# Optimization experiments

Measured on AMD Instinct MI355X. Metric: run time of the kernel, lower is better.

The kernel has to match this reference:

```python
import jax, jax.numpy as jnp
import numpy as np


def _diag_gather(x):
    # out[b,c,h,w] = x[b,c,h,(h+w)%W]; then transpose last two dims and flatten
    B, C, H, W = x.shape
    idx = (jnp.arange(H)[:, None] + jnp.arange(W)[None, :]) % W
    g = jnp.take_along_axis(x, idx[None, None], axis=3)  # [B,C,H,W]
    return g.transpose(0, 1, 3, 2).reshape(B, C, H * W)


def _antidiag_gather(x):
    B, C, H, W = x.shape
    idx = (jnp.arange(W)[None, :] - jnp.arange(H)[:, None]) % W
    g = jnp.take_along_axis(x, idx[None, None], axis=3)
    return g.transpose(0, 1, 3, 2).reshape(B, C, H * W)


def _diag_scatter(flat, shape):
    # exact inverse of _diag_gather (per-row circular-shift permutation)
    B, C, H, W = shape
    t = flat.reshape(B, C, W, H).transpose(0, 1, 3, 2)  # [B,C,H,W]
    inv = (jnp.arange(W)[None, :] - jnp.arange(H)[:, None]) % W
    return jnp.take_along_axis(t, inv[None, None], axis=3)


def _antidiag_scatter(flat, shape):
    B, C, H, W = shape
    t = flat.reshape(B, C, W, H).transpose(0, 1, 3, 2)
    inv = (jnp.arange(W)[None, :] + jnp.arange(H)[:, None]) % W
    return jnp.take_along_axis(t, inv[None, None], axis=3)


def cross_scan(x):
    # x: [B,C,H,W] -> xs: [B,8,C,L]; 8 scan directions (row, col, flips, diag, antidiag, flips)
    B, C, H, W = x.shape
    L = H * W
    xf = x.reshape(B, C, L)
    xt = x.transpose(0, 1, 3, 2).reshape(B, C, L)
    xd = _diag_gather(x)
    xa = _antidiag_gather(x)
    return jnp.stack(
        [xf, xt, xf[..., ::-1], xt[..., ::-1], xd, xa, xd[..., ::-1], xa[..., ::-1]],
        axis=1,
    )


def cross_merge(ys):
    # ys: [B,8,D,H,W] -> y: [B,D,L]
    B, K, D, H, W = ys.shape
    L = H * W
    ys = ys.reshape(B, K, D, L)
    a = ys[:, 0:2] + ys[:, 2:4][..., ::-1]
    y = a[:, 0] + a[:, 1].reshape(B, D, W, H).transpose(0, 1, 3, 2).reshape(B, D, L)
    b = ys[:, 4:6] + ys[:, 6:8][..., ::-1]
    y = y + _diag_scatter(b[:, 0], (B, D, H, W)).reshape(B, D, L)
    y = y + _antidiag_scatter(b[:, 1], (B, D, H, W)).reshape(B, D, L)
    return y


def selective_scan(u, delta, A, Bs, Cs, Ds):
    # u, delta: [B,KD,L]; A: [KD,N]; Bs, Cs: [B,K,N,L]; Ds: [KD]
    Bn, KD, L = u.shape
    K = Bs.shape[1]
    Dd = KD // K
    N = A.shape[1]
    dA = jnp.exp(delta[:, :, None, :] * A[None, :, :, None])  # [B,KD,N,L]
    Bexp = jnp.broadcast_to(Bs[:, :, None], (Bn, K, Dd, N, L)).reshape(Bn, KD, N, L)
    Cexp = jnp.broadcast_to(Cs[:, :, None], (Bn, K, Dd, N, L)).reshape(Bn, KD, N, L)
    dBu = delta[:, :, None, :] * Bexp * u[:, :, None, :]

    def comb(c1, c2):
        a1, b1 = c1
        a2, b2 = c2
        return a2 * a1, a2 * b1 + b2

    _, h = jax.lax.associative_scan(comb, (dA, dBu), axis=-1)  # h: [B,KD,N,L]
    return jnp.sum(Cexp * h, axis=2) + Ds[None, :, None] * u


def setup_inputs() -> dict:
    key = jax.random.key(0)
    ks = jax.random.split(key, 8)
    B, D, H, W = 1, 96, 64, 64
    K, N, R = 8, 16, 6
    return {
        "x": jax.random.normal(ks[0], (B, D, H, W), jnp.float32),
        "x_proj_weight": jax.random.normal(ks[1], (K, R + 2 * N, D), jnp.float32) * 0.05,
        "dt_projs_weight": jax.random.normal(ks[2], (K, D, R), jnp.float32) * 0.1,
        "dt_projs_bias": jax.random.normal(ks[3], (K, D), jnp.float32) * 0.1,
        "A_logs": jax.random.uniform(ks[4], (K * D, N), jnp.float32),
        "Ds": jax.random.normal(ks[5], (K * D,), jnp.float32),
        "out_norm_weight": jnp.ones((D,), jnp.float32),
        "out_norm_bias": jnp.zeros((D,), jnp.float32),
    }


def reference(x, x_proj_weight, dt_projs_weight, dt_projs_bias, A_logs, Ds,
              out_norm_weight, out_norm_bias):
    B, D, H, W = x.shape
    K, _, R = dt_projs_weight.shape
    N = A_logs.shape[1]
    L = H * W

    xs = cross_scan(x)  # [B,K,D,L]
    x_dbl = jnp.einsum("bkdl,kcd->bkcl", xs, x_proj_weight)  # [B,K,R+2N,L]
    dts, Bs, Cs = jnp.split(x_dbl, [R, R + N], axis=2)
    dts = jnp.einsum("bkrl,kdr->bkdl", dts, dt_projs_weight)  # [B,K,D,L]

    u = xs.reshape(B, K * D, L)
    delta = jax.nn.softplus(dts.reshape(B, K * D, L)
                            + dt_projs_bias.reshape(-1)[None, :, None])
    A = -jnp.exp(A_logs)  # [KD,N]

    ys = selective_scan(u, delta, A, Bs, Cs, Ds)  # [B,KD,L]
    y = cross_merge(ys.reshape(B, K, D, H, W))  # [B,D,L]

    # out_norm (v0): LayerNorm over channel dim
    y = y.transpose(0, 2, 1)  # [B,L,D]
    mu = jnp.mean(y, axis=-1, keepdims=True)
    var = jnp.var(y, axis=-1, keepdims=True)
    y = (y - mu) * jax.lax.rsqrt(var + 1e-5) * out_norm_weight + out_norm_bias
    return y.reshape(B, H, W, D)
```

## Files before the change

kernel.cpp:

```cpp
#include <hip/hip_runtime.h>
#include <math.h>

#define D_ 96
#define L_ 4096
#define K_ 8
#define N_ 16
#define R_ 6
#define CDBL 38
#define DL_ (D_ * L_)

#define REPN(M) M(0) M(1) M(2) M(3) M(4) M(5) M(6) M(7) \
                M(8) M(9) M(10) M(11) M(12) M(13) M(14) M(15)
#define REP8(M) M(0) M(1) M(2) M(3) M(4) M(5) M(6) M(7)
#define FENCE asm volatile("" ::: "memory");

#if __has_builtin(__builtin_amdgcn_exp2f)
#define EXP2(x) __builtin_amdgcn_exp2f(x)
#else
#define EXP2(x) exp2f(x)
#endif
#if __has_builtin(__builtin_amdgcn_logf)
#define LOG2F(x) __builtin_amdgcn_logf(x)
#else
#define LOG2F(x) __log2f(x)
#endif

#define LOG2E 1.44269504088896340736f
#define LN2F  0.69314718055994530942f

__device__ __forceinline__ int src_index(int k, int l) {
    int h = l & 63, w = l >> 6;
    int lp = 4095 - l;
    int hp = lp & 63, wp = lp >> 6;
    switch (k) {
    case 0: return l;
    case 1: return (h << 6) + w;
    case 2: return lp;
    case 3: return (hp << 6) + wp;
    case 4: return (h << 6) + ((h + w) & 63);
    case 5: return (h << 6) + ((w - h) & 63);
    case 6: return (hp << 6) + ((hp + wp) & 63);
    default: return (hp << 6) + ((wp - hp) & 63);
    }
}

__global__ __launch_bounds__(256) void k_xdbl(const float* __restrict__ x,
                                              const float* __restrict__ wproj,
                                              float* __restrict__ xdbl) {
    __shared__ float tile[64][100];
    int bid = blockIdx.x;
    int swz = (bid & 7) * 64 + (bid >> 3);
    int k = swz >> 6;
    int l0 = (swz & 63) * 64;

    for (int e = threadIdx.x; e < D_ * 64; e += 256) {
        int d = e >> 6, li = e & 63;
        tile[li][d] = x[d * L_ + src_index(k, l0 + li)];
    }
    __syncthreads();

    int lt = threadIdx.x & 63;
    int cg = __builtin_amdgcn_readfirstlane(threadIdx.x >> 6);
    const float* wk = wproj + k * CDBL * D_;
    float acc[10];
    #pragma unroll
    for (int j = 0; j < 10; ++j) acc[j] = 0.f;
    for (int d4 = 0; d4 < D_; d4 += 4) {
        float4 tv = *(const float4*)&tile[lt][d4];
        #pragma unroll
        for (int j = 0; j < 10; ++j) {
            int c = cg + 4 * j;
            if (c < CDBL) {
                float4 wv = *(const float4*)&wk[c * D_ + d4];
                acc[j] = fmaf(tv.x, wv.x, acc[j]);
                acc[j] = fmaf(tv.y, wv.y, acc[j]);
                acc[j] = fmaf(tv.z, wv.z, acc[j]);
                acc[j] = fmaf(tv.w, wv.w, acc[j]);
            }
        }
    }
    #pragma unroll
    for (int j = 0; j < 10; ++j) {
        int c = cg + 4 * j;
        if (c < CDBL) xdbl[(k * CDBL + c) * L_ + l0 + lt] = acc[j];
    }
}


#if __has_builtin(__builtin_amdgcn_update_dpp)
#define HAVE_DPP 1
template<int CTRL, int RM>
__device__ __forceinline__ float updpp(float oldv, float src) {
    int r = __builtin_amdgcn_update_dpp(__builtin_bit_cast(int, oldv),
                                        __builtin_bit_cast(int, src),
                                        CTRL, RM, 0xF, false);
    return __builtin_bit_cast(float, r);
}
#else
#define HAVE_DPP 0
#endif

__global__ __launch_bounds__(512, 3) void k_scan(const float* __restrict__ xdbl,
                                                 const float* __restrict__ dtw,
                                                 const float* __restrict__ dtb,
                                                 const float* __restrict__ alogs,
                                                 const float* __restrict__ dsv_,
                                                 const float* __restrict__ x,
                                                 float* __restrict__ ys) {
    int bid = blockIdx.x;
    int k = bid & 7;
    int d = bid >> 3;
    int kd = k * D_ + d;
    int t = threadIdx.x;
    int lane = t & 63, wv = t >> 6;
    int l0t = t * 8;

    __shared__ float An_s[16];
    __shared__ float agg_a[8][16], agg_b[8][16];
    __shared__ float cb_s[8][16];
    if (t < 16)
        An_s[t] = -expf(alogs[kd * N_ + t]);

#define DECL(n) float sA##n, sB##n;
    REPN(DECL)
#undef DECL
#define DECL(i) float d##i, u##i, y##i;
    REP8(DECL)
#undef DECL

    const float* xr = xdbl + k * CDBL * L_;
    const float2* wp2 = (const float2*)(dtw + kd * R_);
    const float2 w01 = wp2[0], w23 = wp2[1], w45 = wp2[2];
    const float bias = dtb[kd];
    const float dval = dsv_[kd];
#define SPL2(dst, s) { float p = (s) * LOG2E; \
    float l2 = LOG2F(1.f + EXP2(p)); \
    dst = ((s) > 20.f) ? p : l2; }
#define DLTQ(j, i0, i1, i2, i3) { \
    const float4 r0 = *(const float4*)(xr + 0 * L_ + l0t + j * 4); \
    const float4 r1 = *(const float4*)(xr + 1 * L_ + l0t + j * 4); \
    const float4 r2 = *(const float4*)(xr + 2 * L_ + l0t + j * 4); \
    const float4 r3 = *(const float4*)(xr + 3 * L_ + l0t + j * 4); \
    const float4 r4 = *(const float4*)(xr + 4 * L_ + l0t + j * 4); \
    const float4 r5 = *(const float4*)(xr + 5 * L_ + l0t + j * 4); \
    float s; \
    s = fmaf(w01.x, r0.x, bias); s = fmaf(w01.y, r1.x, s); s = fmaf(w23.x, r2.x, s); \
    s = fmaf(w23.y, r3.x, s); s = fmaf(w45.x, r4.x, s); s = fmaf(w45.y, r5.x, s); \
    SPL2(d##i0, s) \
    s = fmaf(w01.x, r0.y, bias); s = fmaf(w01.y, r1.y, s); s = fmaf(w23.x, r2.y, s); \
    s = fmaf(w23.y, r3.y, s); s = fmaf(w45.x, r4.y, s); s = fmaf(w45.y, r5.y, s); \
    SPL2(d##i1, s) \
    s = fmaf(w01.x, r0.z, bias); s = fmaf(w01.y, r1.z, s); s = fmaf(w23.x, r2.z, s); \
    s = fmaf(w23.y, r3.z, s); s = fmaf(w45.x, r4.z, s); s = fmaf(w45.y, r5.z, s); \
    SPL2(d##i2, s) \
    s = fmaf(w01.x, r0.w, bias); s = fmaf(w01.y, r1.w, s); s = fmaf(w23.x, r2.w, s); \
    s = fmaf(w23.y, r3.w, s); s = fmaf(w45.x, r4.w, s); s = fmaf(w45.y, r5.w, s); \
    SPL2(d##i3, s) }
    DLTQ(0, 0, 1, 2, 3)
    DLTQ(1, 4, 5, 6, 7)
#undef DLTQ
#undef SPL2

    const float* xd = x + d * L_;
#define UG(i) u##i = xd[src_index(k, l0t + i)]; y##i = dval * u##i; \
    u##i *= LN2F; u##i *= d##i;
    REP8(UG)
#undef UG

    __syncthreads();

    const float* Bptr = xdbl + (k * CDBL + R_) * L_ + l0t;
    const float* Cptr = Bptr + N_ * L_;

#define PHA_E(i, Bc) { float e = EXP2(d##i * An); \
    rb = fmaf(e, rb, u##i * (Bc)); ra *= e; }
#define PHA(n) { \
    const float An = An_s[n]; \
    const float* Bn = Bptr + n * L_; \
    const float4 b0 = *(const float4*)(Bn), b1 = *(const float4*)(Bn + 4); \
    float ra = 1.f, rb = 0.f; \
    PHA_E(0, b0.x) PHA_E(1, b0.y) PHA_E(2, b0.z) PHA_E(3, b0.w) \
    PHA_E(4, b1.x) PHA_E(5, b1.y) PHA_E(6, b1.z) PHA_E(7, b1.w) \
    sA##n = ra; sB##n = rb; }
    PHA(0) PHA(1) PHA(2) PHA(3) FENCE
    PHA(4) PHA(5) PHA(6) PHA(7) FENCE
    PHA(8) PHA(9) PHA(10) PHA(11) FENCE
    PHA(12) PHA(13) PHA(14) PHA(15) FENCE
#undef PHA
#undef PHA_E

#if HAVE_DPP
#define SSTN(n) { float pa = updpp<SC_CTRL, SC_RM>(1.f, sA##n); \
                  float pb = updpp<SC_CTRL, SC_RM>(0.f, sB##n); \
                  sB##n = fmaf(sA##n, pb, sB##n); sA##n *= pa; }
#define SC_CTRL 0x111
#define SC_RM 0xF
    REPN(SSTN)
#undef SC_CTRL
#undef SC_RM
#define SC_CTRL 0x112
#define SC_RM 0xF
    REPN(SSTN)
#undef SC_CTRL
#undef SC_RM
#define SC_CTRL 0x114
#define SC_RM 0xF
    REPN(SSTN)
#undef SC_CTRL
#undef SC_RM
#define SC_CTRL 0x118
#define SC_RM 0xF
    REPN(SSTN)
#undef SC_CTRL
#undef SC_RM
#define SC_CTRL 0x142
#define SC_RM 0xA
    REPN(SSTN)
#undef SC_CTRL
#undef SC_RM
#define SC_CTRL 0x143
#define SC_RM 0xC
    REPN(SSTN)
#undef SC_CTRL
#undef SC_RM
#undef SSTN

#define PPREF(n) { \
    if (lane == 63) { agg_a[wv][n] = sA##n; agg_b[wv][n] = sB##n; } \
    sA##n = updpp<0x138, 0xF>(1.f, sA##n); \
    sB##n = updpp<0x138, 0xF>(0.f, sB##n); }
    REPN(PPREF)
#undef PPREF
#else
#define PBF(n) { float pa = __shfl_up(sA##n, off); float pb = __shfl_up(sB##n, off); \
    if (lane >= off) { sB##n = fmaf(sA##n, pb, sB##n); sA##n *= pa; } }
    for (int off = 1; off < 64; off <<= 1) { REPN(PBF) }
#undef PBF
#define PPREF(n) { float ia = sA##n, ib = sB##n; \
    float ea = __shfl_up(ia, 1); float eb = __shfl_up(ib, 1); \
    if (lane == 0) { ea = 1.f; eb = 0.f; } \
    if (lane == 63) { agg_a[wv][n] = ia; agg_b[wv][n] = ib; } \
    sA##n = ea; sB##n = eb; }
    REPN(PPREF)
#undef PPREF
#endif
    __syncthreads();

    if (t < 128) {
        int w = t >> 4, n = t & 15;
        float cb = 0.f;
        for (int w2 = 0; w2 < w; ++w2)
            cb = fmaf(agg_a[w2][n], cb, agg_b[w2][n]);
        cb_s[w][n] = cb;
    }
    __syncthreads();
#define PC(n) { sA##n = fmaf(sA##n, cb_s[wv][n], sB##n); }
    REPN(PC)
#undef PC

#define PHD_E(i, Bc, Cc) { float e = EXP2(d##i * An); \
    h = fmaf(e, h, u##i * (Bc)); y##i = fmaf((Cc), h, y##i); }
#define PHD(n) { \
    const float An = An_s[n]; float h = sA##n; \
    const float* Bn = Bptr + n * L_; const float* Cn = Cptr + n * L_; \
    const float4 b0 = *(const float4*)(Bn), b1 = *(const float4*)(Bn + 4); \
    const float4 c0 = *(const float4*)(Cn), c1 = *(const float4*)(Cn + 4); \
    PHD_E(0, b0.x, c0.x) PHD_E(1, b0.y, c0.y) PHD_E(2, b0.z, c0.z) PHD_E(3, b0.w, c0.w) \
    PHD_E(4, b1.x, c1.x) PHD_E(5, b1.y, c1.y) PHD_E(6, b1.z, c1.z) PHD_E(7, b1.w, c1.w) }
    PHD(0) PHD(1) FENCE
    PHD(2) PHD(3) FENCE
    PHD(4) PHD(5) FENCE
    PHD(6) PHD(7) FENCE
    PHD(8) PHD(9) FENCE
    PHD(10) PHD(11) FENCE
    PHD(12) PHD(13) FENCE
    PHD(14) PHD(15) FENCE
#undef PHD
#undef PHD_E

    float* yp = ys + kd * L_ + l0t;
    {
        float4 o;
        o.x = y0; o.y = y1; o.z = y2; o.w = y3; *(float4*)(yp + 0) = o;
        o.x = y4; o.y = y5; o.z = y6; o.w = y7; *(float4*)(yp + 4) = o;
    }
}

__global__ __launch_bounds__(256) void k_merge_ln(const float* __restrict__ ys,
                                                  const float* __restrict__ gamma,
                                                  const float* __restrict__ beta,
                                                  float* __restrict__ out) {
    __shared__ float sm[32][D_ + 1];
    __shared__ float mu_s[32], rs_s[32];
    int l0 = blockIdx.x * 32;
    for (int e = threadIdx.x; e < 32 * D_; e += 256) {
        int li = e & 31, d = e >> 5;
        int l = l0 + li;
        int h = l >> 6, w = l & 63;
        int i1 = (w << 6) + h;
        int i4 = (((w - h) & 63) << 6) + h;
        int i5 = (((w + h) & 63) << 6) + h;
        const float* bd = ys + d * L_;
        float v = bd[0 * DL_ + l] + bd[2 * DL_ + 4095 - l]
                + bd[1 * DL_ + i1] + bd[3 * DL_ + 4095 - i1]
                + bd[4 * DL_ + i4] + bd[6 * DL_ + 4095 - i4]
                + bd[5 * DL_ + i5] + bd[7 * DL_ + 4095 - i5];
        sm[li][d] = v;
    }
    __syncthreads();
    int li2 = threadIdx.x >> 3, sub = threadIdx.x & 7;
    float s = 0.f, sq = 0.f;
    for (int d = sub; d < D_; d += 8) {
        float v = sm[li2][d];
        s += v; sq = fmaf(v, v, sq);
    }
    s += __shfl_xor(s, 1); sq += __shfl_xor(sq, 1);
    s += __shfl_xor(s, 2); sq += __shfl_xor(sq, 2);
    s += __shfl_xor(s, 4); sq += __shfl_xor(sq, 4);
    if (sub == 0) {
        float mu = s * (1.f / 96.f);
        float var = sq * (1.f / 96.f) - mu * mu;
        mu_s[li2] = mu;
        rs_s[li2] = rsqrtf(var + 1e-5f);
    }
    __syncthreads();
    for (int e = threadIdx.x; e < 32 * D_; e += 256) {
        int li = e / D_, d = e - li * D_;
        float v = (sm[li][d] - mu_s[li]) * rs_s[li];
        out[(l0 + li) * D_ + d] = fmaf(v, gamma[d], beta[d]);
    }
}

extern "C" void kernel_launch(void* const* d_in, const int* in_sizes, int n_in,
                              void* d_out, int out_size, void* d_ws, size_t ws_size,
                              hipStream_t stream) {
    const float* x     = (const float*)d_in[0];
    const float* wproj = (const float*)d_in[1];
    const float* dtw   = (const float*)d_in[2];
    const float* dtb   = (const float*)d_in[3];
    const float* alogs = (const float*)d_in[4];
    const float* dsv   = (const float*)d_in[5];
    const float* gamma = (const float*)d_in[6];
    const float* beta  = (const float*)d_in[7];
    float* out = (float*)d_out;
    float* ws  = (float*)d_ws;

    float* xdbl = ws;
    float* ysb  = ws + 1245184;

    hipLaunchKernelGGL(k_xdbl, dim3(512), dim3(256), 0, stream, x, wproj, xdbl);
    hipLaunchKernelGGL(k_scan, dim3(768), dim3(512), 0, stream,
                       xdbl, dtw, dtb, alogs, dsv, x, ysb);
    hipLaunchKernelGGL(k_merge_ln, dim3(128), dim3(256), 0, stream,
                       ysb, gamma, beta, out);
}
```

Before: 104.0 us.

## Materialize cross-scan via LDS, split scan state in halves, separate merge and layernorm

Adds a k_xscan kernel that stages each channel image in shared memory and writes all eight scan-direction copies contiguously. k_xdbl and k_scan can then read u with coalesced float4 loads instead of scattered gathers. The scan now processes the 16 states in two halves of 8, which lowers register pressure and raises the occupancy hint from 3 to 4. The fused merge+LN kernel is split into an LDS-based merge kernel and a separate LayerNorm kernel. In exchange there are two extra launches and extra global traffic for the xs and ym buffers. k_scan also writes ys in place over xs, which is safe only because each block reads its own row before writing it.

```diff
diff --git a/kernel.cpp b/kernel.cpp
--- a/kernel.cpp
+++ b/kernel.cpp
@@ -9,8 +9,6 @@
 #define CDBL 38
 #define DL_ (D_ * L_)
 
-#define REPN(M) M(0) M(1) M(2) M(3) M(4) M(5) M(6) M(7) \
-                M(8) M(9) M(10) M(11) M(12) M(13) M(14) M(15)
 #define REP8(M) M(0) M(1) M(2) M(3) M(4) M(5) M(6) M(7)
 #define FENCE asm volatile("" ::: "memory");
 
@@ -44,7 +42,49 @@
     }
 }
 
-__global__ __launch_bounds__(256) void k_xdbl(const float* __restrict__ x,
+__device__ __forceinline__ int merge_src(int k, int l) {
+    int h = l >> 6, w = l & 63;
+    int i1 = (w << 6) + h;
+    int i4 = (((w - h) & 63) << 6) + h;
+    int i5 = (((w + h) & 63) << 6) + h;
+    switch (k) {
+    case 0: return l;
+    case 1: return i1;
+    case 2: return 4095 - l;
+    case 3: return 4095 - i1;
+    case 4: return i4;
+    case 5: return i5;
+    case 6: return 4095 - i4;
+    default: return 4095 - i5;
+    }
+}
+
+#define PQ(p) ((((p) >> 6) * 66) + ((p) & 63))
+
+__global__ __launch_bounds__(512) void k_xscan(const float* __restrict__ x,
+                                               float* __restrict__ xs) {
+    __shared__ float img[64 * 66];
+    int d = blockIdx.x;
+    int t = threadIdx.x;
+    const float* xd = x + d * L_;
+    #pragma unroll
+    for (int i = 0; i < 8; ++i) {
+        int l = i * 512 + t;
+        img[PQ(l)] = xd[l];
+    }
+    __syncthreads();
+    #pragma unroll
+    for (int k = 0; k < K_; ++k) {
+        float* dst = xs + (k * D_ + d) * L_;
+        #pragma unroll
+        for (int i = 0; i < 8; ++i) {
+            int l = i * 512 + t;
+            dst[l] = img[PQ(src_index(k, l))];
+        }
+    }
+}
+
+__global__ __launch_bounds__(256) void k_xdbl(const float* __restrict__ xs,
                                               const float* __restrict__ wproj,
                                               float* __restrict__ xdbl) {
     __shared__ float tile[64][100];
@@ -53,9 +93,10 @@
     int k = swz >> 6;
     int l0 = (swz & 63) * 64;
 
+    const float* src = xs + k * DL_ + l0;
     for (int e = threadIdx.x; e < D_ * 64; e += 256) {
         int d = e >> 6, li = e & 63;
-        tile[li][d] = x[d * L_ + src_index(k, l0 + li)];
+        tile[li][d] = src[d * L_ + li];
     }
     __syncthreads();
 
@@ -100,12 +141,12 @@
 #define HAVE_DPP 0
 #endif
 
-__global__ __launch_bounds__(512, 3) void k_scan(const float* __restrict__ xdbl,
+__global__ __launch_bounds__(512, 4) void k_scan(const float* __restrict__ xdbl,
                                                  const float* __restrict__ dtw,
                                                  const float* __restrict__ dtb,
                                                  const float* __restrict__ alogs,
                                                  const float* __restrict__ dsv_,
-                                                 const float* __restrict__ x,
+                                                 const float* __restrict__ xs,
                                                  float* __restrict__ ys) {
     int bid = blockIdx.x;
     int k = bid & 7;
@@ -116,14 +157,13 @@
     int l0t = t * 8;
 
     __shared__ float An_s[16];
-    __shared__ float agg_a[8][16], agg_b[8][16];
-    __shared__ float cb_s[8][16];
+    __shared__ float agg_a[8][8], agg_b[8][8];
+    __shared__ float cb_s[8][8];
     if (t < 16)
         An_s[t] = -expf(alogs[kd * N_ + t]);
 
-#define DECL(n) float sA##n, sB##n;
-    REPN(DECL)
-#undef DECL
+    float sA0, sA1, sA2, sA3, sA4, sA5, sA6, sA7;
+    float sB0, sB1, sB2, sB3, sB4, sB5, sB6, sB7;
 #define DECL(i) float d##i, u##i, y##i;
     REP8(DECL)
 #undef DECL
@@ -161,9 +201,14 @@
 #undef DLTQ
 #undef SPL2
 
-    const float* xd = x + d * L_;
-#define UG(i) u##i = xd[src_index(k, l0t + i)]; y##i = dval * u##i; \
-    u##i *= LN2F; u##i *= d##i;
+    {
+        const float* up = xs + kd * L_ + l0t;
+        const float4 ua = *(const float4*)(up);
+        const float4 ub = *(const float4*)(up + 4);
+        u0 = ua.x; u1 = ua.y; u2 = ua.z; u3 = ua.w;
+        u4 = ub.x; u5 = ub.y; u6 = ub.z; u7 = ub.w;
+    }
+#define UG(i) y##i = dval * u##i; u##i *= LN2F; u##i *= d##i;
     REP8(UG)
 #undef UG
 
@@ -174,109 +219,80 @@
 
 #define PHA_E(i, Bc) { float e = EXP2(d##i * An); \
     rb = fmaf(e, rb, u##i * (Bc)); ra *= e; }
-#define PHA(n) { \
-    const float An = An_s[n]; \
-    const float* Bn = Bptr + n * L_; \
+#define PHA(n, NOFF) { \
+    const float An = An_s[(NOFF) + (n)]; \
+    const float* Bn = Bptr + ((NOFF) + (n)) * L_; \
     const float4 b0 = *(const float4*)(Bn), b1 = *(const float4*)(Bn + 4); \
     float ra = 1.f, rb = 0.f; \
     PHA_E(0, b0.x) PHA_E(1, b0.y) PHA_E(2, b0.z) PHA_E(3, b0.w) \
     PHA_E(4, b1.x) PHA_E(5, b1.y) PHA_E(6, b1.z) PHA_E(7, b1.w) \
     sA##n = ra; sB##n = rb; }
-    PHA(0) PHA(1) PHA(2) PHA(3) FENCE
-    PHA(4) PHA(5) PHA(6) PHA(7) FENCE
-    PHA(8) PHA(9) PHA(10) PHA(11) FENCE
-    PHA(12) PHA(13) PHA(14) PHA(15) FENCE
-#undef PHA
-#undef PHA_E
 
 #if HAVE_DPP
-#define SSTN(n) { float pa = updpp<SC_CTRL, SC_RM>(1.f, sA##n); \
-                  float pb = updpp<SC_CTRL, SC_RM>(0.f, sB##n); \
-                  sB##n = fmaf(sA##n, pb, sB##n); sA##n *= pa; }
-#define SC_CTRL 0x111
-#define SC_RM 0xF
-    REPN(SSTN)
-#undef SC_CTRL
-#undef SC_RM
-#define SC_CTRL 0x112
-#define SC_RM 0xF
-    REPN(SSTN)
-#undef SC_CTRL
-#undef SC_RM
-#define SC_CTRL 0x114
-#define SC_RM 0xF
-    REPN(SSTN)
-#undef SC_CTRL
-#undef SC_RM
-#define SC_CTRL 0x118
-#define SC_RM 0xF
-    REPN(SSTN)
-#undef SC_CTRL
-#undef SC_RM
-#define SC_CTRL 0x142
-#define SC_RM 0xA
-    REPN(SSTN)
-#undef SC_CTRL
-#undef SC_RM
-#define SC_CTRL 0x143
-#define SC_RM 0xC
-    REPN(SSTN)
-#undef SC_CTRL
-#undef SC_RM
-#undef SSTN
-
+#define SSTAGE(CTRL, RM, n) { float pa = updpp<CTRL, RM>(1.f, sA##n); \
+    float pb = updpp<CTRL, RM>(0.f, sB##n); \
+    sB##n = fmaf(sA##n, pb, sB##n); sA##n *= pa; }
+#define SSTAGE8(CTRL, RM) \
+    SSTAGE(CTRL, RM, 0) SSTAGE(CTRL, RM, 1) SSTAGE(CTRL, RM, 2) SSTAGE(CTRL, RM, 3) \
+    SSTAGE(CTRL, RM, 4) SSTAGE(CTRL, RM, 5) SSTAGE(CTRL, RM, 6) SSTAGE(CTRL, RM, 7)
 #define PPREF(n) { \
     if (lane == 63) { agg_a[wv][n] = sA##n; agg_b[wv][n] = sB##n; } \
     sA##n = updpp<0x138, 0xF>(1.f, sA##n); \
     sB##n = updpp<0x138, 0xF>(0.f, sB##n); }
-    REPN(PPREF)
-#undef PPREF
+#define SCAN_CORE \
+    SSTAGE8(0x111, 0xF) SSTAGE8(0x112, 0xF) SSTAGE8(0x114, 0xF) SSTAGE8(0x118, 0xF) \
+    SSTAGE8(0x142, 0xA) SSTAGE8(0x143, 0xC) \
+    REP8(PPREF)
 #else
 #define PBF(n) { float pa = __shfl_up(sA##n, off); float pb = __shfl_up(sB##n, off); \
     if (lane >= off) { sB##n = fmaf(sA##n, pb, sB##n); sA##n *= pa; } }
-    for (int off = 1; off < 64; off <<= 1) { REPN(PBF) }
-#undef PBF
 #define PPREF(n) { float ia = sA##n, ib = sB##n; \
     float ea = __shfl_up(ia, 1); float eb = __shfl_up(ib, 1); \
     if (lane == 0) { ea = 1.f; eb = 0.f; } \
     if (lane == 63) { agg_a[wv][n] = ia; agg_b[wv][n] = ib; } \
     sA##n = ea; sB##n = eb; }
-    REPN(PPREF)
-#undef PPREF
+#define SCAN_CORE \
+    for (int off = 1; off < 64; off <<= 1) { REP8(PBF) } \
+    REP8(PPREF)
 #endif
-    __syncthreads();
-
-    if (t < 128) {
-        int w = t >> 4, n = t & 15;
-        float cb = 0.f;
-        for (int w2 = 0; w2 < w; ++w2)
-            cb = fmaf(agg_a[w2][n], cb, agg_b[w2][n]);
-        cb_s[w][n] = cb;
-    }
-    __syncthreads();
+
 #define PC(n) { sA##n = fmaf(sA##n, cb_s[wv][n], sB##n); }
-    REPN(PC)
-#undef PC
+#define SCAN_MID \
+    SCAN_CORE \
+    __syncthreads(); \
+    if (t < 64) { int cw = t >> 3, cn = t & 7; float cb = 0.f; \
+        for (int w2 = 0; w2 < cw; ++w2) \
+            cb = fmaf(agg_a[w2][cn], cb, agg_b[w2][cn]); \
+        cb_s[cw][cn] = cb; } \
+    __syncthreads(); \
+    REP8(PC)
 
 #define PHD_E(i, Bc, Cc) { float e = EXP2(d##i * An); \
     h = fmaf(e, h, u##i * (Bc)); y##i = fmaf((Cc), h, y##i); }
-#define PHD(n) { \
-    const float An = An_s[n]; float h = sA##n; \
-    const float* Bn = Bptr + n * L_; const float* Cn = Cptr + n * L_; \
+#define PHD(n, NOFF) { \
+    const float An = An_s[(NOFF) + (n)]; float h = sA##n; \
+    const float* Bn = Bptr + ((NOFF) + (n)) * L_; \
+    const float* Cn = Cptr + ((NOFF) + (n)) * L_; \
     const float4 b0 = *(const float4*)(Bn), b1 = *(const float4*)(Bn + 4); \
     const float4 c0 = *(const float4*)(Cn), c1 = *(const float4*)(Cn + 4); \
     PHD_E(0, b0.x, c0.x) PHD_E(1, b0.y, c0.y) PHD_E(2, b0.z, c0.z) PHD_E(3, b0.w, c0.w) \
     PHD_E(4, b1.x, c1.x) PHD_E(5, b1.y, c1.y) PHD_E(6, b1.z, c1.z) PHD_E(7, b1.w, c1.w) }
-    PHD(0) PHD(1) FENCE
-    PHD(2) PHD(3) FENCE
-    PHD(4) PHD(5) FENCE
-    PHD(6) PHD(7) FENCE
-    PHD(8) PHD(9) FENCE
-    PHD(10) PHD(11) FENCE
-    PHD(12) PHD(13) FENCE
-    PHD(14) PHD(15) FENCE
-#undef PHD
-#undef PHD_E
+
+    PHA(0, 0) PHA(1, 0) PHA(2, 0) PHA(3, 0) FENCE
+    PHA(4, 0) PHA(5, 0) PHA(6, 0) PHA(7, 0) FENCE
+    SCAN_MID
+    PHD(0, 0) PHD(1, 0) FENCE
+    PHD(2, 0) PHD(3, 0) FENCE
+    PHD(4, 0) PHD(5, 0) FENCE
+    PHD(6, 0) PHD(7, 0) FENCE
+
+    PHA(0, 8) PHA(1, 8) PHA(2, 8) PHA(3, 8) FENCE
+    PHA(4, 8) PHA(5, 8) PHA(6, 8) PHA(7, 8) FENCE
+    SCAN_MID
+    PHD(0, 8) PHD(1, 8) FENCE
+    PHD(2, 8) PHD(3, 8) FENCE
+    PHD(4, 8) PHD(5, 8) FENCE
+    PHD(6, 8) PHD(7, 8) FENCE
 
     float* yp = ys + kd * L_ + l0t;
     {
@@ -286,48 +302,80 @@
     }
 }
 
-__global__ __launch_bounds__(256) void k_merge_ln(const float* __restrict__ ys,
-                                                  const float* __restrict__ gamma,
-                                                  const float* __restrict__ beta,
-                                                  float* __restrict__ out) {
-    __shared__ float sm[32][D_ + 1];
-    __shared__ float mu_s[32], rs_s[32];
-    int l0 = blockIdx.x * 32;
-    for (int e = threadIdx.x; e < 32 * D_; e += 256) {
-        int li = e & 31, d = e >> 5;
-        int l = l0 + li;
-        int h = l >> 6, w = l & 63;
-        int i1 = (w << 6) + h;
-        int i4 = (((w - h) & 63) << 6) + h;
-        int i5 = (((w + h) & 63) << 6) + h;
-        const float* bd = ys + d * L_;
-        float v = bd[0 * DL_ + l] + bd[2 * DL_ + 4095 - l]
-                + bd[1 * DL_ + i1] + bd[3 * DL_ + 4095 - i1]
-                + bd[4 * DL_ + i4] + bd[6 * DL_ + 4095 - i4]
-                + bd[5 * DL_ + i5] + bd[7 * DL_ + 4095 - i5];
-        sm[li][d] = v;
-    }
-    __syncthreads();
-    int li2 = threadIdx.x >> 3, sub = threadIdx.x & 7;
-    float s = 0.f, sq = 0.f;
-    for (int d = sub; d < D_; d += 8) {
-        float v = sm[li2][d];
-        s += v; sq = fmaf(v, v, sq);
-    }
-    s += __shfl_xor(s, 1); sq += __shfl_xor(sq, 1);
-    s += __shfl_xor(s, 2); sq += __shfl_xor(sq, 2);
-    s += __shfl_xor(s, 4); sq += __shfl_xor(sq, 4);
-    if (sub == 0) {
+__global__ __launch_bounds__(512) void k_merge(const float* __restrict__ ys,
+                                               float* __restrict__ ym) {
+    __shared__ float buf[64 * 66];
+    int d = blockIdx.x;
+    int t = threadIdx.x;
+    float a0 = 0.f, a1 = 0.f, a2 = 0.f, a3 = 0.f,
+          a4 = 0.f, a5 = 0.f, a6 = 0.f, a7 = 0.f;
+    #pragma unroll
+    for (int k = 0; k < K_; ++k) {
+        const float* srow = ys + (k * D_ + d) * L_;
+        #pragma unroll
+        for (int i = 0; i < 8; ++i) {
+            int l = i * 512 + t;
+            buf[PQ(l)] = srow[l];
+        }
+        __syncthreads();
+#define MACC(i) { int l = i * 512 + t; a##i += buf[PQ(merge_src(k, l))]; }
+        REP8(MACC)
+#undef MACC
+        __syncthreads();
+    }
+    float* drow = ym + d * L_;
+#define MST(i) drow[i * 512 + t] = a##i;
+    REP8(MST)
+#undef MST
+}
+
+__global__ __launch_bounds__(512) void k_ln(const float* __restrict__ ym,
+                                            const float* __restrict__ gamma,
+                                            const float* __restrict__ beta,
+                                            float* __restrict__ out) {
+    __shared__ float tile[D_ * 65];
+    __shared__ float pS[8][64], pQ[8][64];
+    __shared__ float mu_s[64], rs_s[64];
+    int t = threadIdx.x;
+    int lb = blockIdx.x * 64;
+
+    #pragma unroll
+    for (int i = 0; i < 12; ++i) {
+        int e = i * 512 + t;
+        int dd = e >> 6, l_loc = e & 63;
+        tile[dd * 65 + l_loc] = ym[dd * L_ + lb + l_loc];
+    }
+    __syncthreads();
+
+    {
+        int wgrp = t >> 6, l_loc = t & 63;
+        float s = 0.f, sq = 0.f;
+        #pragma unroll
+        for (int j = 0; j < 12; ++j) {
+            float v = tile[(wgrp * 12 + j) * 65 + l_loc];
+            s += v; sq = fmaf(v, v, sq);
+        }
+        pS[wgrp][l_loc] = s; pQ[wgrp][l_loc] = sq;
+    }
+    __syncthreads();
+    if (t < 64) {
+        float s = 0.f, sq = 0.f;
+        #pragma unroll
+        for (int w2 = 0; w2 < 8; ++w2) { s += pS[w2][t]; sq += pQ[w2][t]; }
         float mu = s * (1.f / 96.f);
         float var = sq * (1.f / 96.f) - mu * mu;
-        mu_s[li2] = mu;
-        rs_s[li2] = rsqrtf(var + 1e-5f);
-    }
-    __syncthreads();
-    for (int e = threadIdx.x; e < 32 * D_; e += 256) {
-        int li = e / D_, d = e - li * D_;
-        float v = (sm[li][d] - mu_s[li]) * rs_s[li];
-        out[(l0 + li) * D_ + d] = fmaf(v, gamma[d], beta[d]);
+        mu_s[t] = mu;
+        rs_s[t] = rsqrtf(var + 1e-5f);
+    }
+    __syncthreads();
+
+    #pragma unroll
+    for (int i = 0; i < 12; ++i) {
+        int e = i * 512 + t;
+        int l_loc = e / 96, dd = e - l_loc * 96;
+        float v = tile[dd * 65 + l_loc];
+        float o = fmaf((v - mu_s[l_loc]) * rs_s[l_loc], gamma[dd], beta[dd]);
+        out[lb * 96 + e] = o;
     }
 }
 
@@ -345,12 +393,14 @@
     float* out = (float*)d_out;
     float* ws  = (float*)d_ws;
 
-    float* xdbl = ws;
-    float* ysb  = ws + 1245184;
-
-    hipLaunchKernelGGL(k_xdbl, dim3(512), dim3(256), 0, stream, x, wproj, xdbl);
+    float* xs   = ws;
+    float* xdbl = ws + 3145728;
+    float* ym   = ws + 4390912;
+
+    hipLaunchKernelGGL(k_xscan, dim3(96), dim3(512), 0, stream, x, xs);
+    hipLaunchKernelGGL(k_xdbl, dim3(512), dim3(256), 0, stream, xs, wproj, xdbl);
     hipLaunchKernelGGL(k_scan, dim3(768), dim3(512), 0, stream,
-                       xdbl, dtw, dtb, alogs, dsv, x, ysb);
-    hipLaunchKernelGGL(k_merge_ln, dim3(128), dim3(256), 0, stream,
-                       ysb, gamma, beta, out);
-}
+                       xdbl, dtw, dtb, alogs, dsv, xs, xs );
+    hipLaunchKernelGGL(k_merge, dim3(96), dim3(512), 0, stream, xs, ym);
+    hipLaunchKernelGGL(k_ln, dim3(64), dim3(512), 0, stream, ym, gamma, beta, out);
+}
```

Result: slower. 122.5 us (+17.8%).
